# Performance work log

Hardware: AMD Instinct MI355X
Metric: run time of the kernel (lower is better)

Reference implementation:

```python
import jax, jax.numpy as jnp
import numpy as np

N, E, F_IN = 50000, 1_600_000, 256
HID, HEADS, NCLS = 8, 8, 16  # conv1: 8 heads x 8 dims (concat=64); conv2: 1 head -> 16 classes


def setup_inputs() -> dict:
    key = jax.random.key(0)
    ks = jax.random.split(key, 11)
    x = jax.random.normal(ks[0], (N, F_IN), dtype=jnp.float32)
    edge_index = jax.random.randint(ks[1], (2, E), 0, N, dtype=jnp.int32)
    s1 = 1.0 / np.sqrt(F_IN)
    W1 = jax.random.normal(ks[2], (F_IN, HEADS * HID), jnp.float32) * s1
    a_src1 = jax.random.normal(ks[3], (HEADS, HID), jnp.float32) * 0.1
    a_dst1 = jax.random.normal(ks[4], (HEADS, HID), jnp.float32) * 0.1
    b1 = jnp.zeros((HEADS * HID,), jnp.float32)
    s2 = 1.0 / np.sqrt(HEADS * HID)
    W2 = jax.random.normal(ks[5], (HEADS * HID, NCLS), jnp.float32) * s2
    a_src2 = jax.random.normal(ks[6], (1, NCLS), jnp.float32) * 0.1
    a_dst2 = jax.random.normal(ks[7], (1, NCLS), jnp.float32) * 0.1
    b2 = jnp.zeros((NCLS,), jnp.float32)
    return {"x": x, "edge_index": edge_index, "W1": W1, "a_src1": a_src1,
            "a_dst1": a_dst1, "b1": b1, "W2": W2, "a_src2": a_src2,
            "a_dst2": a_dst2, "b2": b2}


def _gat_conv(x, W, a_src, a_dst, bias, src, dst, n, heads, ch, concat):
    # per-head linear transform: [n, heads, ch]
    h = (x @ W).reshape(n, heads, ch)
    # additive attention logits per node, per head
    al_s = jnp.einsum('nhc,hc->nh', h, a_src)
    al_d = jnp.einsum('nhc,hc->nh', h, a_dst)
    e = jax.nn.leaky_relu(al_s[src] + al_d[dst], 0.2)  # [E_tot, heads]
    # segment softmax grouped by destination node (self-loops guarantee non-empty segments)
    m = jax.ops.segment_max(e, dst, num_segments=n)
    ex = jnp.exp(e - m[dst])
    den = jax.ops.segment_sum(ex, dst, num_segments=n)
    alpha = ex / den[dst]  # [E_tot, heads]
    # scatter-aggregate weighted neighbor features
    out = jax.ops.segment_sum(h[src] * alpha[:, :, None], dst, num_segments=n)
    out = out.reshape(n, heads * ch) if concat else out.mean(axis=1)
    return out + bias


def reference(x, edge_index, W1, a_src1, a_dst1, b1, W2, a_src2, a_dst2, b2):
    # add self-loops (PyG GATConv default)
    loops = jnp.arange(N, dtype=edge_index.dtype)
    src = jnp.concatenate([edge_index[0], loops])
    dst = jnp.concatenate([edge_index[1], loops])
    h = _gat_conv(x, W1, a_src1, a_dst1, b1, src, dst, N, HEADS, HID, True)
    h = jax.nn.elu(h)
    out = _gat_conv(h, W2, a_src2, a_dst2, b2, src, dst, N, 1, NCLS, False)
    return jax.nn.log_softmax(out, axis=1)
```

## Files before the change

kernel.cpp:

```cpp
#include <hip/hip_runtime.h>
#include <hip/hip_fp16.h>
#include <hip/hip_fp8.h>

#define NN   50000
#define FIN  256
#define C1   64
#define NH   8
#define NC   16
#define NE   1600000
#define NTOT (NE + NN)

#define CH   256
#define EPC  ((NTOT + CH - 1) / CH)
#define NCB  196
#define GB1  ((NN + 63) / 64)

typedef _Float16 half8 __attribute__((ext_vector_type(8)));
typedef _Float16 half4 __attribute__((ext_vector_type(4)));
typedef float f32x4 __attribute__((ext_vector_type(4)));
typedef float floatx2 __attribute__((ext_vector_type(2)));

#if __has_builtin(__builtin_amdgcn_cvt_pk_f32_fp8) && __has_builtin(__builtin_amdgcn_cvt_pk_fp8_f32)
#define FP8_FAST 1
#endif

__device__ __forceinline__ unsigned pack4_fp8(float f0, float f1, float f2, float f3) {
#ifdef FP8_FAST
    int d = 0;
    d = __builtin_amdgcn_cvt_pk_fp8_f32(f0, f1, d, false);
    d = __builtin_amdgcn_cvt_pk_fp8_f32(f2, f3, d, true);
    return (unsigned)d;
#else
    __hip_fp8_e4m3 q0(f0), q1(f1), q2(f2), q3(f3);
    return (unsigned)q0.__x | ((unsigned)q1.__x << 8) |
           ((unsigned)q2.__x << 16) | ((unsigned)q3.__x << 24);
#endif
}

__device__ __forceinline__ void cvt8_fp8(unsigned lo, unsigned hi, float* f) {
#ifdef FP8_FAST
    floatx2 a = __builtin_amdgcn_cvt_pk_f32_fp8((int)lo, false);
    floatx2 b = __builtin_amdgcn_cvt_pk_f32_fp8((int)lo, true);
    floatx2 c = __builtin_amdgcn_cvt_pk_f32_fp8((int)hi, false);
    floatx2 d = __builtin_amdgcn_cvt_pk_f32_fp8((int)hi, true);
    f[0]=a[0]; f[1]=a[1]; f[2]=b[0]; f[3]=b[1];
    f[4]=c[0]; f[5]=c[1]; f[6]=d[0]; f[7]=d[1];
#else
    #pragma unroll
    for (int u = 0; u < 4; ++u) {
        __hip_fp8_e4m3 q; q.__x = (unsigned char)((lo >> (8*u)) & 0xff);
        f[u] = (float)q;
        __hip_fp8_e4m3 p; p.__x = (unsigned char)((hi >> (8*u)) & 0xff);
        f[4+u] = (float)p;
    }
#endif
}

#define OFF_H1F8  0
#define OFF_G1H   1600000
#define OFF_STAGE 3200000
#define OFF_H2H   3200000
#define OFF_ALS2  3600000
#define OFF_ALD2  3650000
#define OFF_ALS1  6400000
#define OFF_ALD1  6800000
#define OFF_HM    7200000
#define OFF_BASEK 7300352
#define OFF_BTOT  7400704
#define OFF_OFFS  7401600
#define OFF_SRC   7451700

__global__ __launch_bounds__(256) void k_g1rh(const float* __restrict__ x,
                                              const float* __restrict__ W1,
                                              const float* __restrict__ as1,
                                              const float* __restrict__ ad1,
                                              unsigned char* __restrict__ h1f8,
                                              float* __restrict__ als,
                                              float* __restrict__ ald,
                                              const int* __restrict__ ei,
                                              int* __restrict__ H) {
    __shared__ _Float16 wsT[64][264];
    __shared__ int lh[NCB];
    const int tid = threadIdx.x;

    if (blockIdx.x >= GB1) {
        int k = blockIdx.x - GB1;
        for (int i = tid; i < NCB; i += 256) lh[i] = 0;
        __syncthreads();
        int e0 = k * EPC, e1 = min(e0 + EPC, NTOT);
        for (int e = e0 + tid; e < e1; e += 256) {
            int d = (e < NE) ? ei[NE + e] : (e - NE);
            atomicAdd(&lh[d >> 8], 1);
        }
        __syncthreads();
        for (int i = tid; i < NCB; i += 256) H[k * NCB + i] = lh[i];
        return;
    }

    const int r0 = blockIdx.x * 64;
    {
        int c = tid & 63, kb = tid >> 6;
        #pragma unroll
        for (int j = 0; j < 8; ++j) {
            int k8 = kb + 4 * j;
            half8 hv;
            #pragma unroll
            for (int u = 0; u < 8; ++u)
                hv[u] = (_Float16)W1[(size_t)(k8 * 8 + u) * C1 + c];
            *(half8*)(&wsT[c][k8 * 8]) = hv;
        }
    }
    __syncthreads();

    const int lane = tid & 63;
    const int wv   = tid >> 6;
    const int colb = lane & 15;
    const int rgrp = lane >> 4;
    const int arow = r0 + wv * 16 + colb;
    const bool arv = arow < NN;
    f32x4 acc[4] = {};
    #pragma unroll
    for (int s = 0; s < 8; ++s) {
        float4 v0 = make_float4(0.f,0.f,0.f,0.f), v1 = v0;
        if (arv) {
            const float4* xp = (const float4*)(&x[(size_t)arow * FIN + s * 32 + rgrp * 8]);
            v0 = xp[0]; v1 = xp[1];
        }
        half8 a;
        a[0]=(_Float16)v0.x; a[1]=(_Float16)v0.y; a[2]=(_Float16)v0.z; a[3]=(_Float16)v0.w;
        a[4]=(_Float16)v1.x; a[5]=(_Float16)v1.y; a[6]=(_Float16)v1.z; a[7]=(_Float16)v1.w;
        #pragma unroll
        for (int ct = 0; ct < 4; ++ct) {
            half8 b = *(half8*)(&wsT[ct * 16 + colb][s * 32 + rgrp * 8]);
            acc[ct] = __builtin_amdgcn_mfma_f32_16x16x32_f16(a, b, acc[ct], 0, 0, 0);
        }
    }
    __syncthreads();
    _Float16 (*hstore)[72] = (_Float16(*)[72])wsT;
    #pragma unroll
    for (int j = 0; j < 4; ++j) {
        int row = wv * 16 + rgrp * 4 + j;
        #pragma unroll
        for (int ct = 0; ct < 4; ++ct)
            hstore[row][ct * 16 + colb] = (_Float16)acc[ct][j];
    }
    __syncthreads();
    {
        int row = tid >> 2, seg = tid & 3;
        int grow = r0 + row;
        if (grow < NN) {
            half8 h0 = *(half8*)(&hstore[row][seg * 16]);
            half8 h1v = *(half8*)(&hstore[row][seg * 16 + 8]);
            float fv[16];
            #pragma unroll
            for (int u = 0; u < 8; ++u) { fv[u] = (float)h0[u]; fv[8 + u] = (float)h1v[u]; }
            uint4 pk;
            pk.x = pack4_fp8(fv[0],  fv[1],  fv[2],  fv[3]);
            pk.y = pack4_fp8(fv[4],  fv[5],  fv[6],  fv[7]);
            pk.z = pack4_fp8(fv[8],  fv[9],  fv[10], fv[11]);
            pk.w = pack4_fp8(fv[12], fv[13], fv[14], fv[15]);
            *(uint4*)(&h1f8[(size_t)grow * 64 + seg * 16]) = pk;
            float ps0 = 0.f, pd0 = 0.f, ps1 = 0.f, pd1 = 0.f;
            #pragma unroll
            for (int u = 0; u < 8; ++u) {
                ps0 += fv[u]     * as1[seg * 16 + u];
                pd0 += fv[u]     * ad1[seg * 16 + u];
                ps1 += fv[8 + u] * as1[seg * 16 + 8 + u];
                pd1 += fv[8 + u] * ad1[seg * 16 + 8 + u];
            }
            als[grow * NH + seg * 2]     = ps0;
            als[grow * NH + seg * 2 + 1] = ps1;
            ald[grow * NH + seg * 2]     = pd0;
            ald[grow * NH + seg * 2 + 1] = pd1;
        }
    }
}

__global__ __launch_bounds__(256) void k_rsA(const int* __restrict__ H,
                                             int* __restrict__ basek,
                                             int* __restrict__ btot) {
    __shared__ int sc[CH];
    int b = blockIdx.x, t = threadIdx.x;
    int v = H[t * NCB + b];
    sc[t] = v;
    __syncthreads();
    for (int s = 1; s < CH; s <<= 1) {
        int u = (t >= s) ? sc[t - s] : 0;
        __syncthreads();
        sc[t] += u;
        __syncthreads();
    }
    basek[b * CH + t] = sc[t] - v;
    if (t == CH - 1) btot[b] = sc[t];
}

__global__ __launch_bounds__(256) void k_rscatter(const int* __restrict__ ei,
                                                  const int* __restrict__ basek,
                                                  const int* __restrict__ btot,
                                                  int* __restrict__ stage) {
    __shared__ int sc[256];
    __shared__ int lcur[NCB];
    int k = blockIdx.x, t = threadIdx.x;
    int v = (t < NCB) ? btot[t] : 0;
    sc[t] = v;
    __syncthreads();
    for (int s = 1; s < 256; s <<= 1) {
        int u = (t >= s) ? sc[t - s] : 0;
        __syncthreads();
        sc[t] += u;
        __syncthreads();
    }
    if (t < NCB) lcur[t] = (sc[t] - v) + basek[t * CH + k];
    __syncthreads();
    int e0 = k * EPC, e1 = min(e0 + EPC, NTOT);
    for (int e = e0 + t; e < e1; e += 256) {
        int s, d;
        if (e < NE) { s = ei[e]; d = ei[NE + e]; }
        else        { s = e - NE; d = s; }
        int pos = atomicAdd(&lcur[d >> 8], 1);
        stage[pos] = (s << 8) | (d & 255);
    }
}

__global__ __launch_bounds__(256) void k_fsort(const int* __restrict__ stage,
                                               const int* __restrict__ btot,
                                               int* __restrict__ offs,
                                               int* __restrict__ ssrc) {
    __shared__ int sc[256];
    __shared__ int lc[256];
    __shared__ int ls[256];
    __shared__ int lcur[256];
    __shared__ int bb[2];
    int b = blockIdx.x, t = threadIdx.x;
    int v = (t < NCB) ? btot[t] : 0;
    sc[t] = v;
    __syncthreads();
    for (int s = 1; s < 256; s <<= 1) {
        int u = (t >= s) ? sc[t - s] : 0;
        __syncthreads();
        sc[t] += u;
        __syncthreads();
    }
    if (t == b) bb[0] = sc[t] - v;
    if (t == b) bb[1] = sc[t];
    if (b == 0 && t == 0) offs[NN] = NTOT;
    lc[t] = 0;
    __syncthreads();
    int base = bb[0];
    int n = bb[1] - base;
    const int* sp = &stage[base];
    for (int i = t; i < n; i += 256) atomicAdd(&lc[sp[i] & 255], 1);
    __syncthreads();
    int hv = lc[t];
    ls[t] = hv;
    __syncthreads();
    for (int s = 1; s < 256; s <<= 1) {
        int u = (t >= s) ? ls[t - s] : 0;
        __syncthreads();
        ls[t] += u;
        __syncthreads();
    }
    int excl = ls[t] - hv;
    int d = b * 256 + t;
    if (d < NN) offs[d] = base + excl;
    lcur[t] = base + excl;
    __syncthreads();
    for (int i = t; i < n; i += 256) {
        int u = sp[i];
        int pos = atomicAdd(&lcur[u & 255], 1);
        ssrc[pos] = u >> 8;
    }
}

__global__ __launch_bounds__(256) void k_agg1(const int* __restrict__ offs,
                                              const int* __restrict__ src,
                                              const unsigned char* __restrict__ h1f8,
                                              const float* __restrict__ als,
                                              const float* __restrict__ ald,
                                              const float* __restrict__ b1,
                                              _Float16* __restrict__ g1h) {
    int d = blockIdx.x * 4 + (threadIdx.x >> 6);
    if (d >= NN) return;
    const int l = threadIdx.x & 63;
    const int slot = l >> 3, hd = l & 7;
    const unsigned hoff = (unsigned)hd * 4u;
    const unsigned coff = (unsigned)hd * 8u;
    const char* alb = (const char*)als;
    int beg = offs[d], end = offs[d + 1];
    float aldv = ald[d * NH + hd];
    float acc[8] = {};
    float wsum = 0.f;

    for (int r = beg; r < end; r += 16) {
        int e0 = r + slot, e1 = e0 + 8;
        bool v0 = e0 < end, v1 = e1 < end;
        int s0 = src[v0 ? e0 : end - 1];
        int s1 = src[v1 ? e1 : end - 1];
        uint2 q0 = *(const uint2*)(h1f8 + ((unsigned)s0 * 64u + coff));
        uint2 q1 = *(const uint2*)(h1f8 + ((unsigned)s1 * 64u + coff));
        float lg0 = *(const float*)(alb + ((unsigned)s0 * 32u + hoff)) + aldv;
        float lg1 = *(const float*)(alb + ((unsigned)s1 * 32u + hoff)) + aldv;
        lg0 = lg0 > 0.f ? lg0 : 0.2f * lg0;
        lg1 = lg1 > 0.f ? lg1 : 0.2f * lg1;
        float w0 = v0 ? __expf(lg0) : 0.f;
        float w1 = v1 ? __expf(lg1) : 0.f;
        wsum += w0 + w1;
        float f0[8], f1[8];
        cvt8_fp8(q0.x, q0.y, f0);
        cvt8_fp8(q1.x, q1.y, f1);
        #pragma unroll
        for (int u = 0; u < 8; ++u)
            acc[u] += w0 * f0[u] + w1 * f1[u];
    }
    #pragma unroll
    for (int u = 0; u < 8; ++u) {
        acc[u] += __shfl_xor(acc[u], 8);
        acc[u] += __shfl_xor(acc[u], 16);
        acc[u] += __shfl_xor(acc[u], 32);
    }
    wsum += __shfl_xor(wsum, 8);
    wsum += __shfl_xor(wsum, 16);
    wsum += __shfl_xor(wsum, 32);
    if (slot == 0) {
        half8 gv;
        #pragma unroll
        for (int u = 0; u < 8; ++u) {
            float o = acc[u] / wsum + b1[hd * 8 + u];
            o = o > 0.f ? o : (__expf(o) - 1.f);
            gv[u] = (_Float16)o;
        }
        *(half8*)(&g1h[(size_t)d * C1 + hd * 8]) = gv;
    }
}

__global__ __launch_bounds__(256) void k_gemm2(const _Float16* __restrict__ g1h,
                                               const float* __restrict__ W2,
                                               const float* __restrict__ as2,
                                               const float* __restrict__ ad2,
                                               _Float16* __restrict__ h2h,
                                               float* __restrict__ als2,
                                               float* __restrict__ ald2) {
    __shared__ float w2s[C1][17];
    __shared__ _Float16 hact[16][C1 + 8];
    int tid = threadIdx.x;
    for (int i = tid; i < C1 * NC; i += 256) w2s[i >> 4][i & 15] = W2[i];
    int ln = tid >> 4, j = tid & 15;
    int n = blockIdx.x * 16 + ln;
    if (n < NN)
        *(half4*)(&hact[ln][j * 4]) = *(const half4*)(&g1h[(size_t)n * C1 + j * 4]);
    __syncthreads();
    if (n >= NN) return;
    float sum = 0.f;
    #pragma unroll
    for (int c = 0; c < C1; ++c) sum += (float)hact[ln][c] * w2s[c][j];
    h2h[(size_t)n * NC + j] = (_Float16)sum;
    float ps = sum * as2[j], pd = sum * ad2[j];
    #pragma unroll
    for (int w = 1; w < 16; w <<= 1) {
        ps += __shfl_xor(ps, w);
        pd += __shfl_xor(pd, w);
    }
    if (j == 0) { als2[n] = ps; ald2[n] = pd; }
}

__global__ __launch_bounds__(256) void k_agg2(const int* __restrict__ offs,
                                              const int* __restrict__ src,
                                              const _Float16* __restrict__ h2h,
                                              const float* __restrict__ als2,
                                              const float* __restrict__ ald2,
                                              const float* __restrict__ b2,
                                              float* __restrict__ out) {
    int d = blockIdx.x * 4 + (threadIdx.x >> 6);
    if (d >= NN) return;
    const int l = threadIdx.x & 63;
    const int slot = l >> 2, cq = l & 3;
    const unsigned coff = (unsigned)cq * 8u;
    const char* h2b = (const char*)h2h;
    const char* alb = (const char*)als2;
    int beg = offs[d], end = offs[d + 1];
    float aldv = ald2[d];
    float acc[4] = {};
    float wsum = 0.f;
    for (int r = beg; r < end; r += 16) {
        int e = r + slot;
        bool v = e < end;
        int s = src[v ? e : end - 1];
        half4 hv = *(const half4*)(h2b + ((unsigned)s * 32u + coff));
        float lg = *(const float*)(alb + (unsigned)s * 4u) + aldv;
        lg = lg > 0.f ? lg : 0.2f * lg;
        float w = v ? __expf(lg) : 0.f;
        wsum += w;
        #pragma unroll
        for (int u = 0; u < 4; ++u)
            acc[u] += w * (float)hv[u];
    }
    #pragma unroll
    for (int u = 0; u < 4; ++u) {
        acc[u] += __shfl_xor(acc[u], 4);
        acc[u] += __shfl_xor(acc[u], 8);
        acc[u] += __shfl_xor(acc[u], 16);
        acc[u] += __shfl_xor(acc[u], 32);
    }
    wsum += __shfl_xor(wsum, 4);
    wsum += __shfl_xor(wsum, 8);
    wsum += __shfl_xor(wsum, 16);
    wsum += __shfl_xor(wsum, 32);
    float o[4];
    float m = -1e30f;
    #pragma unroll
    for (int u = 0; u < 4; ++u) {
        o[u] = acc[u] / wsum + b2[cq * 4 + u];
        m = fmaxf(m, o[u]);
    }
    m = fmaxf(m, __shfl_xor(m, 1));
    m = fmaxf(m, __shfl_xor(m, 2));
    float sm = 0.f;
    #pragma unroll
    for (int u = 0; u < 4; ++u) sm += __expf(o[u] - m);
    sm += __shfl_xor(sm, 1);
    sm += __shfl_xor(sm, 2);
    float lse = m + __logf(sm);
    if (slot == 0) {
        float4 ov = make_float4(o[0] - lse, o[1] - lse, o[2] - lse, o[3] - lse);
        *(float4*)(&out[(size_t)d * NC + cq * 4]) = ov;
    }
}

extern "C" void kernel_launch(void* const* d_in, const int* in_sizes, int n_in,
                              void* d_out, int out_size, void* d_ws, size_t ws_size,
                              hipStream_t stream) {
    const float* x   = (const float*)d_in[0];
    const int*   ei  = (const int*)  d_in[1];
    const float* W1  = (const float*)d_in[2];
    const float* as1 = (const float*)d_in[3];
    const float* ad1 = (const float*)d_in[4];
    const float* b1  = (const float*)d_in[5];
    const float* W2  = (const float*)d_in[6];
    const float* as2 = (const float*)d_in[7];
    const float* ad2 = (const float*)d_in[8];
    const float* b2  = (const float*)d_in[9];
    float* ws  = (float*)d_ws;
    float* out = (float*)d_out;

    unsigned char* h1f8 = (unsigned char*)(ws + OFF_H1F8);
    _Float16*  g1h  = (_Float16*)(ws + OFF_G1H);
    _Float16*  h2h  = (_Float16*)(ws + OFF_H2H);
    float* als1 = ws + OFF_ALS1;
    float* ald1 = ws + OFF_ALD1;
    float* als2 = ws + OFF_ALS2;
    float* ald2 = ws + OFF_ALD2;
    int* H      = (int*)(ws + OFF_HM);
    int* basek  = (int*)(ws + OFF_BASEK);
    int* btot   = (int*)(ws + OFF_BTOT);
    int* offs   = (int*)(ws + OFF_OFFS);
    int* ssrc   = (int*)(ws + OFF_SRC);
    int* stage  = (int*)(ws + OFF_STAGE);

    k_g1rh    <<<GB1 + CH,       256, 0, stream>>>(x, W1, as1, ad1, h1f8, als1, ald1, ei, H);
    k_rsA     <<<NCB,            256, 0, stream>>>(H, basek, btot);
    k_rscatter<<<CH,             256, 0, stream>>>(ei, basek, btot, stage);
    k_fsort   <<<NCB,            256, 0, stream>>>(stage, btot, offs, ssrc);
    k_agg1    <<<(NN + 3) / 4,   256, 0, stream>>>(offs, ssrc, h1f8, als1, ald1, b1, g1h);
    k_gemm2   <<<(NN + 15) / 16, 256, 0, stream>>>(g1h, W2, as2, ad2, h2h, als2, ald2);
    k_agg2    <<<(NN + 3) / 4,   256, 0, stream>>>(offs, ssrc, h2h, als2, ald2, b2, out);
}
```

Measured before the change: 133.8 us.

## Store layer-1 source logits as fp16, unroll agg1 to four edges, add nontemporal loads

Layer-1 source attention logits are now stored as fp16 in a new workspace region, which halves the bytes fetched per gathered edge in the first aggregation. The agg1 edge loop now handles 32 edges per iteration (four per lane) instead of 16, so more independent gathers are in flight. Streaming reads of edge indices, stage, and sorted src arrays now use nontemporal loads to reduce cache pollution. The fp16 logits lose some precision before the exp, and the extra unrolling raises register pressure and wastes more lanes on low-degree nodes.

```diff
diff --git a/kernel.cpp b/kernel.cpp
--- a/kernel.cpp
+++ b/kernel.cpp
@@ -57,12 +57,12 @@
 }
 
 #define OFF_H1F8  0
+#define OFF_ALS1H 800000
 #define OFF_G1H   1600000
 #define OFF_STAGE 3200000
 #define OFF_H2H   3200000
 #define OFF_ALS2  3600000
 #define OFF_ALD2  3650000
-#define OFF_ALS1  6400000
 #define OFF_ALD1  6800000
 #define OFF_HM    7200000
 #define OFF_BASEK 7300352
@@ -75,7 +75,7 @@
                                               const float* __restrict__ as1,
                                               const float* __restrict__ ad1,
                                               unsigned char* __restrict__ h1f8,
-                                              float* __restrict__ als,
+                                              _Float16* __restrict__ als1h,
                                               float* __restrict__ ald,
                                               const int* __restrict__ ei,
                                               int* __restrict__ H) {
@@ -89,7 +89,7 @@
         __syncthreads();
         int e0 = k * EPC, e1 = min(e0 + EPC, NTOT);
         for (int e = e0 + tid; e < e1; e += 256) {
-            int d = (e < NE) ? ei[NE + e] : (e - NE);
+            int d = (e < NE) ? __builtin_nontemporal_load(&ei[NE + e]) : (e - NE);
             atomicAdd(&lh[d >> 8], 1);
         }
         __syncthreads();
@@ -168,8 +168,8 @@
                 ps1 += fv[8 + u] * as1[seg * 16 + 8 + u];
                 pd1 += fv[8 + u] * ad1[seg * 16 + 8 + u];
             }
-            als[grow * NH + seg * 2]     = ps0;
-            als[grow * NH + seg * 2 + 1] = ps1;
+            als1h[grow * NH + seg * 2]     = (_Float16)ps0;
+            als1h[grow * NH + seg * 2 + 1] = (_Float16)ps1;
             ald[grow * NH + seg * 2]     = pd0;
             ald[grow * NH + seg * 2 + 1] = pd1;
         }
@@ -215,8 +215,10 @@
     int e0 = k * EPC, e1 = min(e0 + EPC, NTOT);
     for (int e = e0 + t; e < e1; e += 256) {
         int s, d;
-        if (e < NE) { s = ei[e]; d = ei[NE + e]; }
-        else        { s = e - NE; d = s; }
+        if (e < NE) {
+            s = __builtin_nontemporal_load(&ei[e]);
+            d = __builtin_nontemporal_load(&ei[NE + e]);
+        } else { s = e - NE; d = s; }
         int pos = atomicAdd(&lcur[d >> 8], 1);
         stage[pos] = (s << 8) | (d & 255);
     }
@@ -249,7 +251,7 @@
     int base = bb[0];
     int n = bb[1] - base;
     const int* sp = &stage[base];
-    for (int i = t; i < n; i += 256) atomicAdd(&lc[sp[i] & 255], 1);
+    for (int i = t; i < n; i += 256) atomicAdd(&lc[__builtin_nontemporal_load(&sp[i]) & 255], 1);
     __syncthreads();
     int hv = lc[t];
     ls[t] = hv;
@@ -266,7 +268,7 @@
     lcur[t] = base + excl;
     __syncthreads();
     for (int i = t; i < n; i += 256) {
-        int u = sp[i];
+        int u = __builtin_nontemporal_load(&sp[i]);
         int pos = atomicAdd(&lcur[u & 255], 1);
         ssrc[pos] = u >> 8;
     }
@@ -275,7 +277,7 @@
 __global__ __launch_bounds__(256) void k_agg1(const int* __restrict__ offs,
                                               const int* __restrict__ src,
                                               const unsigned char* __restrict__ h1f8,
-                                              const float* __restrict__ als,
+                                              const _Float16* __restrict__ als1h,
                                               const float* __restrict__ ald,
                                               const float* __restrict__ b1,
                                               _Float16* __restrict__ g1h) {
@@ -283,34 +285,44 @@
     if (d >= NN) return;
     const int l = threadIdx.x & 63;
     const int slot = l >> 3, hd = l & 7;
-    const unsigned hoff = (unsigned)hd * 4u;
     const unsigned coff = (unsigned)hd * 8u;
-    const char* alb = (const char*)als;
     int beg = offs[d], end = offs[d + 1];
     float aldv = ald[d * NH + hd];
     float acc[8] = {};
     float wsum = 0.f;
 
-    for (int r = beg; r < end; r += 16) {
-        int e0 = r + slot, e1 = e0 + 8;
-        bool v0 = e0 < end, v1 = e1 < end;
-        int s0 = src[v0 ? e0 : end - 1];
-        int s1 = src[v1 ? e1 : end - 1];
+    for (int r = beg; r < end; r += 32) {
+        int e0 = r + slot, e1 = e0 + 8, e2 = e0 + 16, e3 = e0 + 24;
+        bool v0 = e0 < end, v1 = e1 < end, v2 = e2 < end, v3 = e3 < end;
+        int s0 = __builtin_nontemporal_load(&src[v0 ? e0 : end - 1]);
+        int s1 = __builtin_nontemporal_load(&src[v1 ? e1 : end - 1]);
+        int s2 = __builtin_nontemporal_load(&src[v2 ? e2 : end - 1]);
+        int s3 = __builtin_nontemporal_load(&src[v3 ? e3 : end - 1]);
         uint2 q0 = *(const uint2*)(h1f8 + ((unsigned)s0 * 64u + coff));
         uint2 q1 = *(const uint2*)(h1f8 + ((unsigned)s1 * 64u + coff));
-        float lg0 = *(const float*)(alb + ((unsigned)s0 * 32u + hoff)) + aldv;
-        float lg1 = *(const float*)(alb + ((unsigned)s1 * 32u + hoff)) + aldv;
+        uint2 q2 = *(const uint2*)(h1f8 + ((unsigned)s2 * 64u + coff));
+        uint2 q3 = *(const uint2*)(h1f8 + ((unsigned)s3 * 64u + coff));
+        float lg0 = (float)als1h[s0 * NH + hd] + aldv;
+        float lg1 = (float)als1h[s1 * NH + hd] + aldv;
+        float lg2 = (float)als1h[s2 * NH + hd] + aldv;
+        float lg3 = (float)als1h[s3 * NH + hd] + aldv;
         lg0 = lg0 > 0.f ? lg0 : 0.2f * lg0;
         lg1 = lg1 > 0.f ? lg1 : 0.2f * lg1;
+        lg2 = lg2 > 0.f ? lg2 : 0.2f * lg2;
+        lg3 = lg3 > 0.f ? lg3 : 0.2f * lg3;
         float w0 = v0 ? __expf(lg0) : 0.f;
         float w1 = v1 ? __expf(lg1) : 0.f;
-        wsum += w0 + w1;
-        float f0[8], f1[8];
+        float w2 = v2 ? __expf(lg2) : 0.f;
+        float w3 = v3 ? __expf(lg3) : 0.f;
+        wsum += (w0 + w1) + (w2 + w3);
+        float f0[8], f1[8], f2[8], f3[8];
         cvt8_fp8(q0.x, q0.y, f0);
         cvt8_fp8(q1.x, q1.y, f1);
+        cvt8_fp8(q2.x, q2.y, f2);
+        cvt8_fp8(q3.x, q3.y, f3);
         #pragma unroll
         for (int u = 0; u < 8; ++u)
-            acc[u] += w0 * f0[u] + w1 * f1[u];
+            acc[u] += (w0 * f0[u] + w1 * f1[u]) + (w2 * f2[u] + w3 * f3[u]);
     }
     #pragma unroll
     for (int u = 0; u < 8; ++u) {
@@ -384,7 +396,7 @@
     for (int r = beg; r < end; r += 16) {
         int e = r + slot;
         bool v = e < end;
-        int s = src[v ? e : end - 1];
+        int s = __builtin_nontemporal_load(&src[v ? e : end - 1]);
         half4 hv = *(const half4*)(h2b + ((unsigned)s * 32u + coff));
         float lg = *(const float*)(alb + (unsigned)s * 4u) + aldv;
         lg = lg > 0.f ? lg : 0.2f * lg;
@@ -443,9 +455,9 @@
     float* out = (float*)d_out;
 
     unsigned char* h1f8 = (unsigned char*)(ws + OFF_H1F8);
+    _Float16*  als1h = (_Float16*)(ws + OFF_ALS1H);
     _Float16*  g1h  = (_Float16*)(ws + OFF_G1H);
     _Float16*  h2h  = (_Float16*)(ws + OFF_H2H);
-    float* als1 = ws + OFF_ALS1;
     float* ald1 = ws + OFF_ALD1;
     float* als2 = ws + OFF_ALS2;
     float* ald2 = ws + OFF_ALD2;
@@ -456,11 +468,11 @@
     int* ssrc   = (int*)(ws + OFF_SRC);
     int* stage  = (int*)(ws + OFF_STAGE);
 
-    k_g1rh    <<<GB1 + CH,       256, 0, stream>>>(x, W1, as1, ad1, h1f8, als1, ald1, ei, H);
+    k_g1rh    <<<GB1 + CH,       256, 0, stream>>>(x, W1, as1, ad1, h1f8, als1h, ald1, ei, H);
     k_rsA     <<<NCB,            256, 0, stream>>>(H, basek, btot);
     k_rscatter<<<CH,             256, 0, stream>>>(ei, basek, btot, stage);
     k_fsort   <<<NCB,            256, 0, stream>>>(stage, btot, offs, ssrc);
-    k_agg1    <<<(NN + 3) / 4,   256, 0, stream>>>(offs, ssrc, h1f8, als1, ald1, b1, g1h);
+    k_agg1    <<<(NN + 3) / 4,   256, 0, stream>>>(offs, ssrc, h1f8, als1h, ald1, b1, g1h);
     k_gemm2   <<<(NN + 15) / 16, 256, 0, stream>>>(g1h, W2, as2, ad2, h2h, als2, ald2);
     k_agg2    <<<(NN + 3) / 4,   256, 0, stream>>>(offs, ssrc, h2h, als2, ald2, b2, out);
 }
```

Measured after the change: 151.5 us. 1.13x slower.
